# Optimization experiments

Measured on AMD Instinct MI355X. Metric: run time of the kernel, lower is better.

Reference implementation:

```python
import jax, jax.numpy as jnp
import numpy as np

C_LIGHT = 0.299792458  # speed of light in package units
K_U = 2.0 * np.pi      # undulator wavenumber (period = 1.0)


def _field(r, B0):
    # Planar undulator: B = [0, B0*cos(k_u * z), 0]; r: [N,3]
    z = r[..., 2]
    zero = jnp.zeros_like(z)
    return jnp.stack([zero, B0 * jnp.cos(K_U * z), zero], axis=-1)


def _dr_dt(p):
    # dr/dt = p / gamma, gamma = sqrt(1 + |p|^2/c^2)
    gamma = jnp.sqrt(1.0 + jnp.sum(p * p, axis=-1) / C_LIGHT ** 2)
    return p / gamma[..., None]


def _dp_dt(p, field):
    gamma = jnp.sqrt(1.0 + jnp.sum(p * p, axis=-1) / C_LIGHT ** 2)
    return -jnp.cross(p, field, axis=-1) / gamma[..., None]


def setup_inputs() -> dict:
    key = jax.random.key(0)
    k1, k2, k3 = jax.random.split(key, 3)
    N, T = 16384, 1001
    # small transverse offsets around origin
    bunch_r = 0.001 * jax.random.normal(k1, (N, 3), dtype=jnp.float32)
    # directions mostly along +z with small divergence
    d = 0.001 * jax.random.normal(k2, (N, 3), dtype=jnp.float32)
    bunch_d = d.at[:, 2].set(1.0 + d[:, 2])
    # Lorentz factors around 100
    bunch_gamma = 100.0 + 5.0 * jax.random.uniform(k3, (N,), dtype=jnp.float32)
    time = jnp.linspace(0.0, 10.0, T).astype(jnp.float32)
    B0 = jnp.ones((1,), dtype=jnp.float32)
    return {"bunch_r": bunch_r, "bunch_d": bunch_d,
            "bunch_gamma": bunch_gamma, "time": time, "B0": B0}


def reference(bunch_r, bunch_d, bunch_gamma, time, B0):
    b0 = B0[0]
    dt = time[1] - time[0]
    dt2 = dt / 2.0
    n_steps = time.shape[0] - 1

    p0 = (C_LIGHT * jnp.sqrt(bunch_gamma[:, None] ** 2 - 1.0)
          * bunch_d / jnp.linalg.norm(bunch_d, axis=1, keepdims=True))

    def step(state, _):
        r, p = state
        f1 = _field(r, b0)
        rk1 = _dr_dt(p);             pk1 = _dp_dt(p, f1)
        f2 = _field(r + rk1 * dt2, b0)
        rk2 = _dr_dt(p + pk1 * dt2); pk2 = _dp_dt(p + pk1 * dt2, f2)
        f3 = _field(r + rk2 * dt2, b0)
        rk3 = _dr_dt(p + pk2 * dt2); pk3 = _dp_dt(p + pk2 * dt2, f3)
        f4 = _field(r + rk3 * dt, b0)
        rk4 = _dr_dt(p + pk3 * dt);  pk4 = _dp_dt(p + pk3 * dt, f4)
        r_new = r + dt / 6.0 * (rk1 + 2.0 * rk2 + 2.0 * rk3 + rk4)
        p_new = p + dt / 6.0 * (pk1 + 2.0 * pk2 + 2.0 * pk3 + pk4)
        return (r_new, p_new), (r_new, p_new)

    (_, _), (r_hist, p_hist) = jax.lax.scan(step, (bunch_r, p0), None,
                                            length=n_steps)
    # prepend initial state -> [T, N, 3]
    r_all = jnp.concatenate([bunch_r[None], r_hist], axis=0)
    p_all = jnp.concatenate([p0[None], p_hist], axis=0)
    beta_all = p_all / jnp.sqrt(C_LIGHT ** 2
                                + jnp.sum(p_all * p_all, axis=-1))[..., None]
    # [T, N, 3] -> [N, 3, T] matching torch permute((0, 2, 1)) of [N, T, 3]
    bunch_r_out = jnp.transpose(r_all, (1, 2, 0))
    bunch_beta_out = jnp.transpose(beta_all, (1, 2, 0))
    return jnp.stack([bunch_r_out, bunch_beta_out])  # [2, N, 3, T]
```

## Files before the change

### kernel.cpp

```cpp
#include <hip/hip_runtime.h>
#include <math.h>

#define BLOCK 192
#define PPB   64
#define TW    16
#define ROW   385
#define BUFSZ (TW * ROW)
#define SUB   8

#define SYNCW() do {                                              \
    asm volatile("s_waitcnt lgkmcnt(0)" ::: "memory");            \
    __builtin_amdgcn_s_barrier();                                 \
    asm volatile("" ::: "memory");                                \
} while (0)

#if defined(__has_builtin)
# if __has_builtin(__builtin_amdgcn_cosf) && __has_builtin(__builtin_amdgcn_fractf)
#  define COS2PI(x) __builtin_amdgcn_cosf(__builtin_amdgcn_fractf(x))
# endif
#endif
#ifndef COS2PI
# define COS2PI(x) __cosf(6.283185307179586f * (x))
#endif

__global__ __launch_bounds__(BLOCK) void track_rk4(
    const float* __restrict__ r_in,
    const float* __restrict__ d_vec,
    const float* __restrict__ g_in,
    const float* __restrict__ t_in,
    const float* __restrict__ b_in,
    float* __restrict__ out,
    int N, int T)
{
    __shared__ float L[2 * BUFSZ];

    const int tid    = threadIdx.x;
    const int wid    = tid >> 6;
    const int lane   = tid & 63;
    const int blockP = blockIdx.x * PPB;

    const long Tl     = (long)T;
    const long boff   = 3L * (long)N * Tl;
    const int  ntiles = (T + TW - 1) / TW;

    const float c      = 0.299792458f;
    const float inv_c2 = 1.0f / (c * c);
    const float inv_c  = 1.0f / c;

    const float b0  = b_in[0];
    const float dt  = t_in[1] - t_in[0];

    if (wid == 0) {
        float rx = 0.f, ry = 0.f, rz = 0.f, px = 0.f, py = 0.f, pz = 0.f;
        const int n0 = blockP + lane;
        if (n0 < N) {
            rx = r_in[3*n0+0]; ry = r_in[3*n0+1]; rz = r_in[3*n0+2];
            const float dx = d_vec[3*n0+0], dy = d_vec[3*n0+1], dz = d_vec[3*n0+2];
            const float g0 = g_in[n0];
            const float pscale = c * sqrtf(g0*g0 - 1.0f)
                               * rsqrtf(fmaf(dx,dx, fmaf(dy,dy, dz*dz)));
            px = dx * pscale; py = dy * pscale; pz = dz * pscale;
        }

        const float p2s    = fmaf(px,px, fmaf(py,py, pz*pz));
        const float ig     = rsqrtf(fmaf(p2s, inv_c2, 1.0f));
        const float H      = dt * (float)SUB;
        const float igH2   = ig * (0.5f * H);
        const float igH    = ig * H;
        const float bigH2  = b0 * igH2;
        const float igH6   = ig * H * (1.0f / 6.0f);
        const float dry    = py * ig * dt;
        const float bscale = ig * inv_c;
        const float byv    = py * bscale;
        const float bigHb  = b0 * igH * bscale;

        float cy = COS2PI(rz);

        float e_rx=0.f, m_rx=0.f, a_rx=0.f, b_rx=0.f;
        float e_rz=0.f, m_rz=0.f, a_rz=0.f, b_rz=0.f;
        float e_bx=0.f, m_bx=0.f, a_bx=0.f, b_bx=0.f;
        float e_bz=0.f, m_bz=0.f, a_bz=0.f, b_bz=0.f;
        float ry0e = 0.f;

        const int pi = ((lane & 3) << 4) | (lane >> 2);

        for (int tile = 0; tile <= ntiles; ++tile) {
            if (tile < ntiles) {
                float* __restrict__ Lw = &L[(tile & 1) * BUFSZ + pi];
                const int t0 = tile * TW;
                #pragma unroll
                for (int tt = 0; tt < TW; ++tt) {
                    const int tg = t0 + tt;
                    if (tg < T) {
                        float orx, oryv, orz, obx, obz;
                        if (tg == 0) {
                            orx = rx; oryv = ry; orz = rz;
                            obx = px * bscale; obz = pz * bscale;
                        } else {
                            const int k = (tt + 7) & 7;
                            if (k == 0) {
                                const float g1  = cy * bigH2;
                                const float z2  = fmaf(pz, igH2, rz);
                                const float c2v = COS2PI(z2);
                                const float q1x = pz * g1,  q1z = px * g1;
                                const float p2x = px + q1x, p2z = pz - q1z;

                                const float g2  = c2v * bigH2;
                                const float z3  = fmaf(p2z, igH2, rz);
                                const float c3v = COS2PI(z3);
                                const float q2x = p2z * g2, q2z = p2x * g2;
                                const float p3x = px + q2x, p3z = pz - q2z;

                                const float g3  = c3v * bigH2;
                                const float z4  = fmaf(p3z, igH, rz);
                                const float c4v = COS2PI(z4);
                                const float q3x = p3z * g3, q3z = p3x * g3;
                                const float p4x = fmaf(q3x,  2.0f, px);
                                const float p4z = fmaf(q3z, -2.0f, pz);

                                const float g4  = c4v * bigH2;
                                const float q4x = p4z * g4, q4z = p4x * g4;

                                const float ax = px + p4x, bx = p2x + p3x;
                                const float az = pz + p4z, bz = p2z + p3z;
                                const float rx1 = fmaf(fmaf(bx, 2.0f, ax), igH6, rx);
                                const float rz1 = fmaf(fmaf(bz, 2.0f, az), igH6, rz);
                                const float sx = q1x + q4x, tx = q2x + q3x;
                                const float sz = q1z + q4z, tz = q2z + q3z;
                                const float px1 = fmaf(fmaf(tx, 2.0f, sx),  (1.0f/3.0f), px);
                                const float pz1 = fmaf(fmaf(tz, 2.0f, sz), (-1.0f/3.0f), pz);
                                const float cy1 = COS2PI(rz1);

                                { const float m0 = px*igH, m1 = px1*igH, dd = rx1 - rx;
                                  e_rx = rx; m_rx = m0;
                                  a_rx = fmaf(3.0f, dd, -(m0+m0+m1));
                                  b_rx = (m0+m1) - (dd+dd); }
                                { const float m0 = pz*igH, m1 = pz1*igH, dd = rz1 - rz;
                                  e_rz = rz; m_rz = m0;
                                  a_rz = fmaf(3.0f, dd, -(m0+m0+m1));
                                  b_rz = (m0+m1) - (dd+dd); }
                                { const float y0 = px*bscale, y1 = px1*bscale;
                                  const float m0 = (cy*pz)*bigHb, m1 = (cy1*pz1)*bigHb;
                                  const float dd = y1 - y0;
                                  e_bx = y0; m_bx = m0;
                                  a_bx = fmaf(3.0f, dd, -(m0+m0+m1));
                                  b_bx = (m0+m1) - (dd+dd); }
                                { const float y0 = pz*bscale, y1 = pz1*bscale;
                                  const float m0 = -(cy*px)*bigHb, m1 = -(cy1*px1)*bigHb;
                                  const float dd = y1 - y0;
                                  e_bz = y0; m_bz = m0;
                                  a_bz = fmaf(3.0f, dd, -(m0+m0+m1));
                                  b_bz = (m0+m1) - (dd+dd); }
                                ry0e = ry;
                                ry   = fmaf((float)SUB, dry, ry);
                                rx = rx1; rz = rz1; px = px1; pz = pz1; cy = cy1;
                            }
                            const float tau = (float)(k + 1) * (1.0f / (float)SUB);
                            orx  = fmaf(tau, fmaf(tau, fmaf(tau, b_rx, a_rx), m_rx), e_rx);
                            orz  = fmaf(tau, fmaf(tau, fmaf(tau, b_rz, a_rz), m_rz), e_rz);
                            obx  = fmaf(tau, fmaf(tau, fmaf(tau, b_bx, a_bx), m_bx), e_bx);
                            obz  = fmaf(tau, fmaf(tau, fmaf(tau, b_bz, a_bz), m_bz), e_bz);
                            oryv = fmaf((float)(k + 1), dry, ry0e);
                        }
                        Lw[tt*ROW + 0*64] = orx;
                        Lw[tt*ROW + 1*64] = oryv;
                        Lw[tt*ROW + 2*64] = orz;
                        Lw[tt*ROW + 3*64] = obx;
                        Lw[tt*ROW + 4*64] = byv;
                        Lw[tt*ROW + 5*64] = obz;
                    }
                }
            }
            SYNCW();
        }
    } else {
        const int g = lane >> 4;
        const int e = lane & 15;
        const int c6base = 3 * (wid - 1);
        const int rbase  = e * ROW + c6base * 64 + g * 16;
        const long pstride = 3L * Tl;

        float* bp[3];
        #pragma unroll
        for (int j = 0; j < 3; ++j) {
            const int  c6  = c6base + j;
            const int  c6m = (c6 < 3) ? c6 : c6 - 3;
            const long sel = (c6 < 3) ? 0L : boff;
            bp[j] = out + sel + (3L*(blockP + g) + c6m) * Tl + e;
        }
        const int pbmax = N - blockP - g;

        for (int tile = 0; tile <= ntiles; ++tile) {
            if (tile > 0) {
                const int dtile = tile - 1;
                const float* __restrict__ Lb = &L[(dtile & 1) * BUFSZ];
                const int t0  = dtile * TW;
                const int rem = (T - t0 < TW) ? (T - t0) : TW;
                const bool on = (e < rem);
                #pragma unroll
                for (int j = 0; j < 3; ++j) {
                    float v[16];
                    #pragma unroll
                    for (int i = 0; i < 16; ++i)
                        v[i] = Lb[rbase + j*64 + i];
                    #pragma unroll
                    for (int i = 0; i < 16; ++i) {
                        const int pb = i * 4;
                        if (on && pb < pbmax)
                            bp[j][(long)t0 + pb * pstride] = v[i];
                    }
                }
            }
            SYNCW();
        }
    }
}

extern "C" void kernel_launch(void* const* d_in, const int* in_sizes, int n_in,
                              void* d_out, int out_size, void* d_ws, size_t ws_size,
                              hipStream_t stream) {
    const float* r  = (const float*)d_in[0];
    const float* d  = (const float*)d_in[1];
    const float* g  = (const float*)d_in[2];
    const float* tm = (const float*)d_in[3];
    const float* b0 = (const float*)d_in[4];
    float* out = (float*)d_out;

    const int N = in_sizes[2];
    const int T = in_sizes[3];

    const int blocks = (N + PPB - 1) / PPB;
    track_rk4<<<blocks, BLOCK, 0, stream>>>(r, d, g, tm, b0, out, N, T);
}
```

Before: 587.0 us.

## Align writer-wave output stores to 64B segments with carried partial chunks

```diff
diff --git a/kernel.cpp b/kernel.cpp
--- a/kernel.cpp
+++ b/kernel.cpp
@@ -3,7 +3,7 @@
 
 #define BLOCK 192
 #define PPB   64
-#define TW    16
+#define TW    32
 #define ROW   385
 #define BUFSZ (TW * ROW)
 #define SUB   8
@@ -177,37 +177,72 @@
         const int g = lane >> 4;
         const int e = lane & 15;
         const int c6base = 3 * (wid - 1);
-        const int rbase  = e * ROW + c6base * 64 + g * 16;
-        const long pstride = 3L * Tl;
-
-        float* bp[3];
+        const long pstride  = 3L * Tl;
+        const long pstride4 = 4L * pstride;
+
+        float* bp0[3];
+        int    Sj[3];
         #pragma unroll
         for (int j = 0; j < 3; ++j) {
-            const int  c6  = c6base + j;
-            const int  c6m = (c6 < 3) ? c6 : c6 - 3;
+            const int c6  = c6base + j;
+            const int c6m = (c6 < 3) ? c6 : c6 - 3;
             const long sel = (c6 < 3) ? 0L : boff;
-            bp[j] = out + sel + (3L*(blockP + g) + c6m) * Tl + e;
+            bp0[j] = out + sel + (3L*(blockP + g) + c6m) * Tl;
+            Sj[j]  = 3*(blockP + g) + c6m;
         }
         const int pbmax = N - blockP - g;
+
+        float carry[3][16];
+        #pragma unroll
+        for (int j = 0; j < 3; ++j)
+            #pragma unroll
+            for (int i = 0; i < 16; ++i) carry[j][i] = 0.f;
 
         for (int tile = 0; tile <= ntiles; ++tile) {
             if (tile > 0) {
                 const int dtile = tile - 1;
                 const float* __restrict__ Lb = &L[(dtile & 1) * BUFSZ];
-                const int t0  = dtile * TW;
-                const int rem = (T - t0 < TW) ? (T - t0) : TW;
-                const bool on = (e < rem);
+                const bool lastz = (dtile >= ntiles - 2);
                 #pragma unroll
                 for (int j = 0; j < 3; ++j) {
-                    float v[16];
-                    #pragma unroll
-                    for (int i = 0; i < 16; ++i)
-                        v[i] = Lb[rbase + j*64 + i];
+                    const int cofs = (c6base + j) * 64 + (g << 4);
+                    float fC[16], f2[16];
                     #pragma unroll
                     for (int i = 0; i < 16; ++i) {
-                        const int pb = i * 4;
-                        if (on && pb < pbmax)
-                            bp[j][(long)t0 + pb * pstride] = v[i];
+                        const int h  = (7 * Sj[j] + 4 * (i & 3)) & 15;
+                        const int qC = h + e;
+                        const int q2 = (h + e + 16) & 31;
+                        fC[i] = Lb[qC * ROW + cofs + i];
+                        f2[i] = Lb[q2 * ROW + cofs + i];
+                    }
+                    __builtin_amdgcn_sched_barrier(0);
+                    #pragma unroll
+                    for (int i = 0; i < 16; ++i) {
+                        const int h  = (7 * Sj[j] + 4 * (i & 3)) & 15;
+                        const int Li = (T - h) >> 4;
+                        const int kB = 2 * dtile - 1;
+                        const int kC = 2 * dtile;
+                        float* sp = bp0[j] + (long)i * pstride4;
+                        const bool okp = (4 * i < pbmax);
+                        if (okp) {
+                            if (dtile == 0) {
+                                if (e >= 16 - h)
+                                    sp[h + e - 16] = f2[i];
+                            } else if (kB < Li) {
+                                sp[h + 16 * kB + e] =
+                                    (e < 16 - h) ? carry[j][i] : f2[i];
+                            }
+                            if (kC < Li)
+                                sp[h + 16 * kC + e] = fC[i];
+                            if (lastz) {
+                                const int ts = h + 16 * Li;
+                                const int tC = TW * dtile + (h + e);
+                                const int t2 = TW * dtile + ((h + e + 16) & 31);
+                                if (tC >= ts && tC < T) sp[tC] = fC[i];
+                                if (t2 >= ts && t2 < T) sp[t2] = f2[i];
+                            }
+                        }
+                        carry[j][i] = (e < 16 - h) ? f2[i] : carry[j][i];
                     }
                 }
             }
```

New measurement: 541.0 us. 7.8% less time.

## Restructure writer warps to emit aligned float4 stores with cross-tile carry

Applied to the files above, without the earlier changes.

```diff
diff --git a/kernel.cpp b/kernel.cpp
--- a/kernel.cpp
+++ b/kernel.cpp
@@ -1,12 +1,14 @@
 #include <hip/hip_runtime.h>
 #include <math.h>
 
-#define BLOCK 192
+#define BLOCK 320
 #define PPB   64
-#define TW    16
+#define TW    32
 #define ROW   385
 #define BUFSZ (TW * ROW)
 #define SUB   8
+
+typedef float f4 __attribute__((ext_vector_type(4)));
 
 #define SYNCW() do {                                              \
     asm volatile("s_waitcnt lgkmcnt(0)" ::: "memory");            \
@@ -174,40 +176,76 @@
             SYNCW();
         }
     } else {
-        const int g = lane >> 4;
-        const int e = lane & 15;
-        const int c6base = 3 * (wid - 1);
-        const int rbase  = e * ROW + c6base * 64 + g * 16;
-        const long pstride = 3L * Tl;
-
-        float* bp[3];
+        const int w  = wid - 1;
+        const int is = lane >> 2;
+        const int q  = lane & 3;
+        const int p  = 4 * is + w;
+        const bool okp = (p < N - blockP);
+
+        float* bpp[6]; int hh[6]; int colv[6]; int Liv[6];
         #pragma unroll
-        for (int j = 0; j < 3; ++j) {
-            const int  c6  = c6base + j;
+        for (int c6 = 0; c6 < 6; ++c6) {
             const int  c6m = (c6 < 3) ? c6 : c6 - 3;
             const long sel = (c6 < 3) ? 0L : boff;
-            bp[j] = out + sel + (3L*(blockP + g) + c6m) * Tl + e;
-        }
-        const int pbmax = N - blockP - g;
+            const int  S   = 3*(blockP + p) + c6m;
+            const int  h   = (7 * S) & 15;
+            hh[c6]   = h;
+            Liv[c6]  = (T - h) >> 4;
+            colv[c6] = c6*64 + (w << 4) + is;
+            bpp[c6]  = out + sel + (long)S * Tl + h + 4*q;
+        }
+
+        f4 carry[6];
+        #pragma unroll
+        for (int c6 = 0; c6 < 6; ++c6)
+            #pragma unroll
+            for (int mm = 0; mm < 4; ++mm) carry[c6][mm] = 0.f;
 
         for (int tile = 0; tile <= ntiles; ++tile) {
             if (tile > 0) {
-                const int dtile = tile - 1;
-                const float* __restrict__ Lb = &L[(dtile & 1) * BUFSZ];
-                const int t0  = dtile * TW;
-                const int rem = (T - t0 < TW) ? (T - t0) : TW;
-                const bool on = (e < rem);
+                const int d = tile - 1;
+                const float* __restrict__ Lb = &L[(d & 1) * BUFSZ];
+                const int kB = 2*d - 1, kC = 2*d;
+                const bool lastz = (d >= ntiles - 2);
                 #pragma unroll
-                for (int j = 0; j < 3; ++j) {
-                    float v[16];
+                for (int c6 = 0; c6 < 6; ++c6) {
+                    const int h = hh[c6], col = colv[c6], Li = Liv[c6];
+                    f4 vC, vB;
                     #pragma unroll
-                    for (int i = 0; i < 16; ++i)
-                        v[i] = Lb[rbase + j*64 + i];
-                    #pragma unroll
-                    for (int i = 0; i < 16; ++i) {
-                        const int pb = i * 4;
-                        if (on && pb < pbmax)
-                            bp[j][(long)t0 + pb * pstride] = v[i];
+                    for (int mm = 0; mm < 4; ++mm) {
+                        const int m  = 4*q + mm;
+                        const float fC = Lb[(h + m)*ROW + col];
+                        const float f2 = Lb[((16 + h + m) & 31)*ROW + col];
+                        const bool lo  = (m < 16 - h);
+                        vC[mm] = fC;
+                        vB[mm] = lo ? carry[c6][mm] : f2;
+                        carry[c6][mm] = lo ? f2 : carry[c6][mm];
+                    }
+                    if (okp) {
+                        if (d == 0) {
+                            #pragma unroll
+                            for (int mm = 0; mm < 4; ++mm) {
+                                const int m = 4*q + mm;
+                                if (m >= 16 - h) bpp[c6][mm - 16] = vB[mm];
+                            }
+                        } else if (kB < Li) {
+                            *reinterpret_cast<f4*>(bpp[c6] + 16L*kB) = vB;
+                        }
+                        if (kC < Li)
+                            *reinterpret_cast<f4*>(bpp[c6] + 16L*kC) = vC;
+                        if (lastz) {
+                            float* tb = bpp[c6] - h - 4*q;
+                            const int tmin = h + 16*Li;
+                            #pragma unroll
+                            for (int u = 0; u < 2; ++u)
+                                #pragma unroll
+                                for (int mm = 0; mm < 4; ++mm) {
+                                    const int r = 16*u + 4*q + mm;
+                                    const int t = TW*d + r;
+                                    if (t >= tmin && t < T)
+                                        tb[t] = Lb[r*ROW + col];
+                                }
+                        }
                     }
                 }
             }
```

New measurement: 477.0 us. 18.7% less time.
